# Performance work log

Measured on AMD Instinct MI355X. Metric: run time of the kernel, lower is better.

Reference implementation:

```python
import jax, jax.numpy as jnp
import numpy as np

B, S, D_IN, D_OUT = 4, 2048, 1024, 1024


def setup_inputs() -> dict:
    key = jax.random.key(0)
    kx, kq, kk, kv = jax.random.split(key, 4)
    scale = 1.0 / np.sqrt(D_IN)
    return {
        "x": jax.random.normal(kx, (B, S, D_IN), dtype=jnp.float32),
        "W_q": jax.random.normal(kq, (D_IN, D_OUT), dtype=jnp.float32) * scale,
        "W_k": jax.random.normal(kk, (D_IN, D_OUT), dtype=jnp.float32) * scale,
        "W_v": jax.random.normal(kv, (D_IN, D_OUT), dtype=jnp.float32) * scale,
    }


def reference(x, W_q, W_k, W_v):
    # QKV projections (Linear without bias): [B,S,D_out]
    q = jnp.einsum("bsd,de->bse", x, W_q)
    k = jnp.einsum("bsd,de->bse", x, W_k)
    v = jnp.einsum("bsd,de->bse", x, W_v)

    # Raw scores [B,S,S], causal mask (strict upper triangle -> -inf),
    # then scale by sqrt(d_k) and softmax, matching the torch order of ops.
    scores = jnp.einsum("bqd,bkd->bqk", q, k)
    seq = scores.shape[-1]
    causal = jnp.triu(jnp.ones((seq, seq), dtype=bool), k=1)
    scores = jnp.where(causal[None, :, :], -jnp.inf, scores)
    attn = jax.nn.softmax(scores / jnp.sqrt(jnp.asarray(q.shape[-1], scores.dtype)), axis=-1)
    # dropout p=0.0 -> identity (eval semantics)
    return jnp.einsum("bqk,bkd->bqd", attn, v)
```

## Files before the change

### kernel.cpp

```cpp
#include <hip/hip_runtime.h>

typedef unsigned short u16;
typedef __bf16 bf16x8 __attribute__((ext_vector_type(8)));
typedef float f32x4 __attribute__((ext_vector_type(4)));

__device__ __forceinline__ u16 f2bf(float f) {
    union { float f; unsigned int u; } v; v.f = f;
    unsigned int u = v.u;
    return (u16)((u + 0x7FFFu + ((u >> 16) & 1u)) >> 16);
}

__device__ __forceinline__ void load_lds16(const void* g, void* l) {
    __builtin_amdgcn_global_load_lds(
        (const __attribute__((address_space(1))) unsigned int*)g,
        (__attribute__((address_space(3))) unsigned int*)l,
        16, 0, 0);
}

__global__ void __launch_bounds__(256) prep_kernel(
    const float4* __restrict__ X, u16* __restrict__ xb,
    const float* __restrict__ Wq, const float* __restrict__ Wk,
    const float* __restrict__ Wv,
    u16* __restrict__ Oq, u16* __restrict__ Ok, u16* __restrict__ Ov,
    float* __restrict__ rowsum) {
    __shared__ float tile[32][33];
    const int bid = blockIdx.x, tid = threadIdx.x;
    if (bid < 8192) {
        int idx = bid * 256 + tid;
        float4 v = X[idx];
        ushort4 o;
        o.x = f2bf(v.x); o.y = f2bf(v.y); o.z = f2bf(v.z); o.w = f2bf(v.w);
        *(ushort4*)(xb + (size_t)idx * 4) = o;
    } else if (bid < 11264) {
        int id = bid - 8192;
        int zz = id >> 10;
        const float* W = (zz == 0) ? Wq : (zz == 1) ? Wk : Wv;
        u16* O = (zz == 0) ? Oq : (zz == 1) ? Ok : Ov;
        int n0 = (id & 31) * 32, k0 = ((id >> 5) & 31) * 32;
        int tx = tid & 31, ty = tid >> 5;
        #pragma unroll
        for (int j = 0; j < 32; j += 8)
            tile[ty + j][tx] = W[(size_t)(k0 + ty + j) * 1024 + n0 + tx];
        __syncthreads();
        #pragma unroll
        for (int j = 0; j < 32; j += 8)
            O[(size_t)(n0 + ty + j) * 1024 + k0 + tx] = f2bf(tile[tx][ty + j]);
    } else {
        rowsum[(bid - 11264) * 256 + tid] = 0.f;
    }
}

__global__ void __launch_bounds__(512) gemm_qkv(
    const u16* __restrict__ xb, const u16* __restrict__ WqT,
    const u16* __restrict__ WkT, const u16* __restrict__ WvT,
    u16* __restrict__ Q, u16* __restrict__ Kb, u16* __restrict__ Vt) {

    int L = blockIdx.x;
    int c = L & 7, t = (L >> 3) & 7, hi = L >> 6;
    int p = hi * 8 + c;
    const int z = p >> 6, mtile = p & 63, ntile = t;
    const u16* A = xb;
    const u16* B = (z == 0) ? WqT : (z == 1) ? WkT : WvT;

    __shared__ __align__(16) u16 As[2 * 128 * 32];
    __shared__ __align__(16) u16 Bs[2 * 128 * 32];

    const int tid = threadIdx.x;
    const int lane = tid & 63;
    const int wave = tid >> 6;
    const int wr = wave >> 2, wc = wave & 3;

    const int r0 = tid >> 2;
    const int kb = (((tid & 3) ^ ((r0 >> 1) & 3))) * 16;

    const char* gA = (const char*)(A + (size_t)(mtile * 128 + r0) * 1024) + kb;
    const char* gB = (const char*)(B + (size_t)(ntile * 128 + r0) * 1024) + kb;
    char* lA = (char*)As + tid * 16;
    char* lB = (char*)Bs + tid * 16;

    f32x4 acc[4][2] = {};

    const int quad = lane >> 4;
    const int l16 = lane & 15;
    const int ch = quad ^ ((l16 >> 1) & 3);
    const int aoff = (wr * 64 + l16) * 32 + ch * 8;
    const int boff = (wc * 32 + l16) * 32 + ch * 8;

    for (int kt = 0; kt < 16; ++kt) {
        load_lds16(gA,      lA);
        load_lds16(gA + 64, lA + 8192);
        load_lds16(gB,      lB);
        load_lds16(gB + 64, lB + 8192);
        gA += 128; gB += 128;
        __syncthreads();
        #pragma unroll
        for (int h = 0; h < 2; ++h) {
            const u16* ap = As + h * 4096 + aoff;
            const u16* bp = Bs + h * 4096 + boff;
            bf16x8 af[4], bfv[2];
            #pragma unroll
            for (int r = 0; r < 4; ++r) af[r] = *(const bf16x8*)(ap + r * 512);
            #pragma unroll
            for (int cc = 0; cc < 2; ++cc) bfv[cc] = *(const bf16x8*)(bp + cc * 512);
            #pragma unroll
            for (int r = 0; r < 4; ++r)
                #pragma unroll
                for (int cc = 0; cc < 2; ++cc)
                    acc[r][cc] = __builtin_amdgcn_mfma_f32_16x16x32_bf16(
                        af[r], bfv[cc], acc[r][cc], 0, 0, 0);
        }
        __syncthreads();
    }

    const int grow0 = mtile * 128 + wr * 64 + quad * 4;
    const int gcol0 = ntile * 128 + wc * 32 + l16;

    if (z < 2) {
        u16* C = z ? Kb : Q;
        #pragma unroll
        for (int r = 0; r < 4; ++r)
            #pragma unroll
            for (int cc = 0; cc < 2; ++cc)
                #pragma unroll
                for (int i = 0; i < 4; ++i)
                    C[(size_t)(grow0 + r * 16 + i) * 1024 + gcol0 + cc * 16] =
                        f2bf(acc[r][cc][i]);
    } else {
        #pragma unroll
        for (int r = 0; r < 4; ++r) {
            int m0 = grow0 + r * 16;
            int b = m0 >> 11, s0 = m0 & 2047;
            #pragma unroll
            for (int cc = 0; cc < 2; ++cc) {
                int d = gcol0 + cc * 16;
                ushort4 o;
                o.x = f2bf(acc[r][cc][0]); o.y = f2bf(acc[r][cc][1]);
                o.z = f2bf(acc[r][cc][2]); o.w = f2bf(acc[r][cc][3]);
                *(ushort4*)(Vt + (size_t)b * (1024 * 2048) + (size_t)d * 2048 + s0) = o;
            }
        }
    }
}

__global__ void __launch_bounds__(512) gemm_scores(
    const u16* __restrict__ Q, const u16* __restrict__ Kb,
    u16* __restrict__ S, float* __restrict__ rowsum) {

    const int L = blockIdx.x;
    const int c = L & 7;
    const int q = L >> 3;
    const int z = q / 17;
    const int j = q - z * 17;
    const int mtile = (j <= c) ? c : 15 - c;
    const int ntile = (j <= c) ? j : j - c - 1;

    const u16* A = Q  + (size_t)z * (2048 * 1024);
    const u16* B = Kb + (size_t)z * (2048 * 1024);

    __shared__ __align__(16) u16 As[2 * 128 * 32];
    __shared__ __align__(16) u16 Bs[2 * 128 * 32];

    const int tid = threadIdx.x;
    const int lane = tid & 63;
    const int wave = tid >> 6;
    const int wr = wave >> 2, wc = wave & 3;

    const int r0 = tid >> 2;
    const int kb = (((tid & 3) ^ ((r0 >> 1) & 3))) * 16;

    const char* gA = (const char*)(A + (size_t)(mtile * 128 + r0) * 1024) + kb;
    const char* gB = (const char*)(B + (size_t)(ntile * 128 + r0) * 1024) + kb;
    char* lA = (char*)As + tid * 16;
    char* lB = (char*)Bs + tid * 16;

    f32x4 acc[4][2] = {};

    const int quad = lane >> 4;
    const int l16 = lane & 15;
    const int ch = quad ^ ((l16 >> 1) & 3);
    const int aoff = (wr * 64 + l16) * 32 + ch * 8;
    const int boff = (wc * 32 + l16) * 32 + ch * 8;

    for (int kt = 0; kt < 16; ++kt) {
        load_lds16(gA,      lA);
        load_lds16(gA + 64, lA + 8192);
        load_lds16(gB,      lB);
        load_lds16(gB + 64, lB + 8192);
        gA += 128; gB += 128;
        __syncthreads();
        #pragma unroll
        for (int h = 0; h < 2; ++h) {
            const u16* ap = As + h * 4096 + aoff;
            const u16* bp = Bs + h * 4096 + boff;
            bf16x8 af[4], bfv[2];
            #pragma unroll
            for (int r = 0; r < 4; ++r) af[r] = *(const bf16x8*)(ap + r * 512);
            #pragma unroll
            for (int cc = 0; cc < 2; ++cc) bfv[cc] = *(const bf16x8*)(bp + cc * 512);
            #pragma unroll
            for (int r = 0; r < 4; ++r)
                #pragma unroll
                for (int cc = 0; cc < 2; ++cc)
                    acc[r][cc] = __builtin_amdgcn_mfma_f32_16x16x32_bf16(
                        af[r], bfv[cc], acc[r][cc], 0, 0, 0);
        }
        __syncthreads();
    }

    const int grow0 = mtile * 128 + wr * 64 + quad * 4;
    const int gcol0 = ntile * 128 + wc * 32 + l16;

    u16* C = S + (size_t)z * (2048 * 2048);
    float* rs = rowsum + z * 2048;
    const bool diag = (ntile == mtile);
    float rsum[4][4];
    #pragma unroll
    for (int r = 0; r < 4; ++r)
        #pragma unroll
        for (int i = 0; i < 4; ++i) rsum[r][i] = 0.f;
    #pragma unroll
    for (int r = 0; r < 4; ++r)
        #pragma unroll
        for (int cc = 0; cc < 2; ++cc)
            #pragma unroll
            for (int i = 0; i < 4; ++i) {
                int grow = grow0 + r * 16 + i;
                int gcol = gcol0 + cc * 16;
                float e = 0.f;
                if (!diag || gcol <= grow)
                    e = __expf(acc[r][cc][i] * 0.03125f - 12.0f);
                C[(size_t)grow * 2048 + gcol] = f2bf(e);
                rsum[r][i] += e;
            }
    #pragma unroll
    for (int r = 0; r < 4; ++r)
        #pragma unroll
        for (int i = 0; i < 4; ++i) {
            float s = rsum[r][i];
            s += __shfl_xor(s, 1, 64);
            s += __shfl_xor(s, 2, 64);
            s += __shfl_xor(s, 4, 64);
            s += __shfl_xor(s, 8, 64);
            if (l16 == 0)
                atomicAdd(&rs[grow0 + r * 16 + i], s);
        }
}

__global__ void __launch_bounds__(512) gemm_pv(
    const u16* __restrict__ S, const u16* __restrict__ Vt,
    const float* __restrict__ rowsum, float* __restrict__ out) {

    const int L = blockIdx.x;
    const int ntile = L & 7;
    const int x = L >> 3;
    const int z = x & 3;
    const int mp = x >> 2;

    const u16* Abase = S  + (size_t)z * (2048 * 2048);
    const u16* B     = Vt + (size_t)z * (1024 * 2048);
    const float* rs  = rowsum + z * 2048;
    float* C = out + (size_t)z * (2048 * 1024);

    __shared__ __align__(16) u16 As[2 * 128 * 32];
    __shared__ __align__(16) u16 Bs[2 * 128 * 32];

    const int tid = threadIdx.x;
    const int lane = tid & 63;
    const int wave = tid >> 6;
    const int wr = wave >> 2, wc = wave & 3;

    const int r0 = tid >> 2;
    const int kb = (((tid & 3) ^ ((r0 >> 1) & 3))) * 16;

    char* lA = (char*)As + tid * 16;
    char* lB = (char*)Bs + tid * 16;

    const int quad = lane >> 4;
    const int l16 = lane & 15;
    const int ch = quad ^ ((l16 >> 1) & 3);
    const int aoff = (wr * 64 + l16) * 32 + ch * 8;
    const int boff = (wc * 32 + l16) * 32 + ch * 8;

    #pragma unroll
    for (int ti = 0; ti < 2; ++ti) {
        const int mtile = ti ? mp : 15 - mp;
        const int kiters = (mtile + 1) * 2;

        const char* gA = (const char*)(Abase + (size_t)(mtile * 128 + r0) * 2048) + kb;
        const char* gB = (const char*)(B + (size_t)(ntile * 128 + r0) * 2048) + kb;

        f32x4 acc[4][2] = {};

        for (int kt = 0; kt < kiters; ++kt) {
            load_lds16(gA,      lA);
            load_lds16(gA + 64, lA + 8192);
            load_lds16(gB,      lB);
            load_lds16(gB + 64, lB + 8192);
            gA += 128; gB += 128;
            __syncthreads();
            #pragma unroll
            for (int h = 0; h < 2; ++h) {
                const u16* ap = As + h * 4096 + aoff;
                const u16* bp = Bs + h * 4096 + boff;
                bf16x8 af[4], bfv[2];
                #pragma unroll
                for (int r = 0; r < 4; ++r) af[r] = *(const bf16x8*)(ap + r * 512);
                #pragma unroll
                for (int cc = 0; cc < 2; ++cc) bfv[cc] = *(const bf16x8*)(bp + cc * 512);
                #pragma unroll
                for (int r = 0; r < 4; ++r)
                    #pragma unroll
                    for (int cc = 0; cc < 2; ++cc)
                        acc[r][cc] = __builtin_amdgcn_mfma_f32_16x16x32_bf16(
                            af[r], bfv[cc], acc[r][cc], 0, 0, 0);
            }
            __syncthreads();
        }

        const int grow0 = mtile * 128 + wr * 64 + quad * 4;
        const int gcol0 = ntile * 128 + wc * 32 + l16;
        #pragma unroll
        for (int r = 0; r < 4; ++r)
            #pragma unroll
            for (int i = 0; i < 4; ++i) {
                int grow = grow0 + r * 16 + i;
                float inv = 1.0f / rs[grow];
                #pragma unroll
                for (int cc = 0; cc < 2; ++cc)
                    C[(size_t)grow * 1024 + gcol0 + cc * 16] = acc[r][cc][i] * inv;
            }
    }
}

extern "C" void kernel_launch(void* const* d_in, const int* in_sizes, int n_in,
                              void* d_out, int out_size, void* d_ws, size_t ws_size,
                              hipStream_t stream) {
    const float* x  = (const float*)d_in[0];
    const float* Wq = (const float*)d_in[1];
    const float* Wk = (const float*)d_in[2];
    const float* Wv = (const float*)d_in[3];
    float* out = (float*)d_out;
    char* ws = (char*)d_ws;
    const size_t Mi = 1u << 20;

    u16* xb  = (u16*)(ws);
    u16* WqT = (u16*)(ws + 16 * Mi);
    u16* WkT = (u16*)(ws + 18 * Mi);
    u16* WvT = (u16*)(ws + 20 * Mi);
    u16* Q   = (u16*)(ws + 22 * Mi);
    u16* Kb  = (u16*)(ws + 38 * Mi);
    u16* Vt  = (u16*)(ws + 54 * Mi);
    u16* S   = (u16*)(ws + 70 * Mi);
    float* rowsum = (float*)(ws + 102 * Mi);

    prep_kernel<<<11296, 256, 0, stream>>>(
        (const float4*)x, xb, Wq, Wk, Wv, WqT, WkT, WvT, rowsum);

    gemm_qkv<<<1536, 512, 0, stream>>>(xb, WqT, WkT, WvT, Q, Kb, Vt);

    gemm_scores<<<544, 512, 0, stream>>>(Q, Kb, S, rowsum);

    gemm_pv<<<256, 512, 0, stream>>>(S, Vt, rowsum, out);
}
```

Measured before the change: 225.1 us.

## Split score and PV GEMMs into 128x64 tiles with heavy-first causal scheduling

Both attention GEMMs now use 256-thread blocks that each compute a 128x64 output tile, replacing 512-thread blocks with 128x128 tiles. This raises the block count from 544/256 to 1088/1024. The PV kernel no longer pairs a short and a long causal row-tile in one block; it launches one block per tile, ordered from the longest K range down, so the hardware scheduler balances the load. The aim is better CU occupancy and less tail imbalance, at the cost of reloading each A tile twice and extra per-block overhead.

```diff
diff --git a/kernel.cpp b/kernel.cpp
--- a/kernel.cpp
+++ b/kernel.cpp
@@ -142,34 +142,36 @@
     }
 }
 
-__global__ void __launch_bounds__(512) gemm_scores(
+__global__ void __launch_bounds__(256) gemm_scores(
     const u16* __restrict__ Q, const u16* __restrict__ Kb,
     u16* __restrict__ S, float* __restrict__ rowsum) {
 
     const int L = blockIdx.x;
     const int c = L & 7;
     const int q = L >> 3;
-    const int z = q / 17;
-    const int j = q - z * 17;
-    const int mtile = (j <= c) ? c : 15 - c;
-    const int ntile = (j <= c) ? j : j - c - 1;
+    const int z = q / 34;
+    const int j = q - z * 34;
+    int mtile, nh;
+    if (j < 2 * (c + 1)) { mtile = c;      nh = j; }
+    else                 { mtile = 15 - c; nh = j - 2 * (c + 1); }
 
     const u16* A = Q  + (size_t)z * (2048 * 1024);
     const u16* B = Kb + (size_t)z * (2048 * 1024);
 
     __shared__ __align__(16) u16 As[2 * 128 * 32];
-    __shared__ __align__(16) u16 Bs[2 * 128 * 32];
+    __shared__ __align__(16) u16 Bs[2 * 64 * 32];
 
     const int tid = threadIdx.x;
     const int lane = tid & 63;
     const int wave = tid >> 6;
-    const int wr = wave >> 2, wc = wave & 3;
+    const int wr = wave >> 1, wc = wave & 1;
 
     const int r0 = tid >> 2;
     const int kb = (((tid & 3) ^ ((r0 >> 1) & 3))) * 16;
 
-    const char* gA = (const char*)(A + (size_t)(mtile * 128 + r0) * 1024) + kb;
-    const char* gB = (const char*)(B + (size_t)(ntile * 128 + r0) * 1024) + kb;
+    const char* gA0 = (const char*)(A + (size_t)(mtile * 128 + r0) * 1024) + kb;
+    const char* gA1 = gA0 + (size_t)64 * 1024 * 2;
+    const char* gB  = (const char*)(B + (size_t)(nh * 64 + r0) * 1024) + kb;
     char* lA = (char*)As + tid * 16;
     char* lB = (char*)Bs + tid * 16;
 
@@ -182,16 +184,18 @@
     const int boff = (wc * 32 + l16) * 32 + ch * 8;
 
     for (int kt = 0; kt < 16; ++kt) {
-        load_lds16(gA,      lA);
-        load_lds16(gA + 64, lA + 8192);
-        load_lds16(gB,      lB);
-        load_lds16(gB + 64, lB + 8192);
-        gA += 128; gB += 128;
+        #pragma unroll
+        for (int h = 0; h < 2; ++h) {
+            load_lds16(gA0 + h * 64, lA + h * 8192);
+            load_lds16(gA1 + h * 64, lA + 4096 + h * 8192);
+            load_lds16(gB  + h * 64, lB + h * 4096);
+        }
+        gA0 += 128; gA1 += 128; gB += 128;
         __syncthreads();
         #pragma unroll
         for (int h = 0; h < 2; ++h) {
             const u16* ap = As + h * 4096 + aoff;
-            const u16* bp = Bs + h * 4096 + boff;
+            const u16* bp = Bs + h * 2048 + boff;
             bf16x8 af[4], bfv[2];
             #pragma unroll
             for (int r = 0; r < 4; ++r) af[r] = *(const bf16x8*)(ap + r * 512);
@@ -208,11 +212,10 @@
     }
 
     const int grow0 = mtile * 128 + wr * 64 + quad * 4;
-    const int gcol0 = ntile * 128 + wc * 32 + l16;
+    const int gcol0 = nh * 64 + wc * 32 + l16;
 
     u16* C = S + (size_t)z * (2048 * 2048);
     float* rs = rowsum + z * 2048;
-    const bool diag = (ntile == mtile);
     float rsum[4][4];
     #pragma unroll
     for (int r = 0; r < 4; ++r)
@@ -226,9 +229,9 @@
             for (int i = 0; i < 4; ++i) {
                 int grow = grow0 + r * 16 + i;
                 int gcol = gcol0 + cc * 16;
-                float e = 0.f;
-                if (!diag || gcol <= grow)
-                    e = __expf(acc[r][cc][i] * 0.03125f - 12.0f);
+                float e = (gcol <= grow)
+                              ? __expf(acc[r][cc][i] * 0.03125f - 12.0f)
+                              : 0.f;
                 C[(size_t)grow * 2048 + gcol] = f2bf(e);
                 rsum[r][i] += e;
             }
@@ -246,34 +249,42 @@
         }
 }
 
-__global__ void __launch_bounds__(512) gemm_pv(
+__global__ void __launch_bounds__(256) gemm_pv(
     const u16* __restrict__ S, const u16* __restrict__ Vt,
     const float* __restrict__ rowsum, float* __restrict__ out) {
 
     const int L = blockIdx.x;
-    const int ntile = L & 7;
-    const int x = L >> 3;
-    const int z = x & 3;
-    const int mp = x >> 2;
-
-    const u16* Abase = S  + (size_t)z * (2048 * 2048);
-    const u16* B     = Vt + (size_t)z * (1024 * 2048);
-    const float* rs  = rowsum + z * 2048;
+    const int c = L & 7;
+    const int z = c >> 1;
+    const int nhhi = c & 1;
+    const int j = L >> 3;
+    const int mtile = 15 - (j >> 3);
+    const int nh = nhhi * 8 + (j & 7);
+    const int kiters = (mtile + 1) * 2;
+
+    const u16* A = S  + (size_t)z * (2048 * 2048);
+    const u16* B = Vt + (size_t)z * (1024 * 2048);
+    const float* rs = rowsum + z * 2048;
     float* C = out + (size_t)z * (2048 * 1024);
 
     __shared__ __align__(16) u16 As[2 * 128 * 32];
-    __shared__ __align__(16) u16 Bs[2 * 128 * 32];
+    __shared__ __align__(16) u16 Bs[2 * 64 * 32];
 
     const int tid = threadIdx.x;
     const int lane = tid & 63;
     const int wave = tid >> 6;
-    const int wr = wave >> 2, wc = wave & 3;
+    const int wr = wave >> 1, wc = wave & 1;
 
     const int r0 = tid >> 2;
     const int kb = (((tid & 3) ^ ((r0 >> 1) & 3))) * 16;
 
+    const char* gA0 = (const char*)(A + (size_t)(mtile * 128 + r0) * 2048) + kb;
+    const char* gA1 = gA0 + (size_t)64 * 2048 * 2;
+    const char* gB  = (const char*)(B + (size_t)(nh * 64 + r0) * 2048) + kb;
     char* lA = (char*)As + tid * 16;
     char* lB = (char*)Bs + tid * 16;
+
+    f32x4 acc[4][2] = {};
 
     const int quad = lane >> 4;
     const int l16 = lane & 15;
@@ -281,55 +292,46 @@
     const int aoff = (wr * 64 + l16) * 32 + ch * 8;
     const int boff = (wc * 32 + l16) * 32 + ch * 8;
 
-    #pragma unroll
-    for (int ti = 0; ti < 2; ++ti) {
-        const int mtile = ti ? mp : 15 - mp;
-        const int kiters = (mtile + 1) * 2;
-
-        const char* gA = (const char*)(Abase + (size_t)(mtile * 128 + r0) * 2048) + kb;
-        const char* gB = (const char*)(B + (size_t)(ntile * 128 + r0) * 2048) + kb;
-
-        f32x4 acc[4][2] = {};
-
-        for (int kt = 0; kt < kiters; ++kt) {
-            load_lds16(gA,      lA);
-            load_lds16(gA + 64, lA + 8192);
-            load_lds16(gB,      lB);
-            load_lds16(gB + 64, lB + 8192);
-            gA += 128; gB += 128;
-            __syncthreads();
-            #pragma unroll
-            for (int h = 0; h < 2; ++h) {
-                const u16* ap = As + h * 4096 + aoff;
-                const u16* bp = Bs + h * 4096 + boff;
-                bf16x8 af[4], bfv[2];
-                #pragma unroll
-                for (int r = 0; r < 4; ++r) af[r] = *(const bf16x8*)(ap + r * 512);
-                #pragma unroll
-                for (int cc = 0; cc < 2; ++cc) bfv[cc] = *(const bf16x8*)(bp + cc * 512);
-                #pragma unroll
-                for (int r = 0; r < 4; ++r)
-                    #pragma unroll
-                    for (int cc = 0; cc < 2; ++cc)
-                        acc[r][cc] = __builtin_amdgcn_mfma_f32_16x16x32_bf16(
-                            af[r], bfv[cc], acc[r][cc], 0, 0, 0);
-            }
-            __syncthreads();
-        }
-
-        const int grow0 = mtile * 128 + wr * 64 + quad * 4;
-        const int gcol0 = ntile * 128 + wc * 32 + l16;
-        #pragma unroll
-        for (int r = 0; r < 4; ++r)
-            #pragma unroll
-            for (int i = 0; i < 4; ++i) {
-                int grow = grow0 + r * 16 + i;
-                float inv = 1.0f / rs[grow];
+    for (int kt = 0; kt < kiters; ++kt) {
+        #pragma unroll
+        for (int h = 0; h < 2; ++h) {
+            load_lds16(gA0 + h * 64, lA + h * 8192);
+            load_lds16(gA1 + h * 64, lA + 4096 + h * 8192);
+            load_lds16(gB  + h * 64, lB + h * 4096);
+        }
+        gA0 += 128; gA1 += 128; gB += 128;
+        __syncthreads();
+        #pragma unroll
+        for (int h = 0; h < 2; ++h) {
+            const u16* ap = As + h * 4096 + aoff;
+            const u16* bp = Bs + h * 2048 + boff;
+            bf16x8 af[4], bfv[2];
+            #pragma unroll
+            for (int r = 0; r < 4; ++r) af[r] = *(const bf16x8*)(ap + r * 512);
+            #pragma unroll
+            for (int cc = 0; cc < 2; ++cc) bfv[cc] = *(const bf16x8*)(bp + cc * 512);
+            #pragma unroll
+            for (int r = 0; r < 4; ++r)
                 #pragma unroll
                 for (int cc = 0; cc < 2; ++cc)
-                    C[(size_t)grow * 1024 + gcol0 + cc * 16] = acc[r][cc][i] * inv;
-            }
-    }
+                    acc[r][cc] = __builtin_amdgcn_mfma_f32_16x16x32_bf16(
+                        af[r], bfv[cc], acc[r][cc], 0, 0, 0);
+        }
+        __syncthreads();
+    }
+
+    const int grow0 = mtile * 128 + wr * 64 + quad * 4;
+    const int gcol0 = nh * 64 + wc * 32 + l16;
+    #pragma unroll
+    for (int r = 0; r < 4; ++r)
+        #pragma unroll
+        for (int i = 0; i < 4; ++i) {
+            int grow = grow0 + r * 16 + i;
+            float inv = 1.0f / rs[grow];
+            #pragma unroll
+            for (int cc = 0; cc < 2; ++cc)
+                C[(size_t)grow * 1024 + gcol0 + cc * 16] = acc[r][cc][i] * inv;
+        }
 }
 
 extern "C" void kernel_launch(void* const* d_in, const int* in_sizes, int n_in,
@@ -358,7 +360,7 @@
 
     gemm_qkv<<<1536, 512, 0, stream>>>(xb, WqT, WkT, WvT, Q, Kb, Vt);
 
-    gemm_scores<<<544, 512, 0, stream>>>(Q, Kb, S, rowsum);
-
-    gemm_pv<<<256, 512, 0, stream>>>(S, Vt, rowsum, out);
-}
+    gemm_scores<<<1088, 256, 0, stream>>>(Q, Kb, S, rowsum);
+
+    gemm_pv<<<1024, 256, 0, stream>>>(S, Vt, rowsum, out);
+}
```

Result: slower. 232.4 us (+3.2%).

## Move V projection into the scores kernel to balance launch work

Applied to the files above, without the earlier changes.

The V projection tiles are split out of the QKV GEMM and launched in the same grid as the causal score GEMM, so a single launch covers 544 score tiles plus 512 V tiles. The goal is to fill the GPU better, since the score kernel alone has only 544 blocks and a ragged tail, and to shrink the first GEMM. The cost is a heterogeneous kernel with branches on block type. Scores still depend on Q and K from the previous launch, which the ordering keeps intact.

```diff
diff --git a/kernel.cpp b/kernel.cpp
--- a/kernel.cpp
+++ b/kernel.cpp
@@ -50,17 +50,17 @@
     }
 }
 
-__global__ void __launch_bounds__(512) gemm_qkv(
+__global__ void __launch_bounds__(512) gemm_qk(
     const u16* __restrict__ xb, const u16* __restrict__ WqT,
-    const u16* __restrict__ WkT, const u16* __restrict__ WvT,
-    u16* __restrict__ Q, u16* __restrict__ Kb, u16* __restrict__ Vt) {
+    const u16* __restrict__ WkT,
+    u16* __restrict__ Q, u16* __restrict__ Kb) {
 
     int L = blockIdx.x;
     int c = L & 7, t = (L >> 3) & 7, hi = L >> 6;
     int p = hi * 8 + c;
     const int z = p >> 6, mtile = p & 63, ntile = t;
     const u16* A = xb;
-    const u16* B = (z == 0) ? WqT : (z == 1) ? WkT : WvT;
+    const u16* B = z ? WkT : WqT;
 
     __shared__ __align__(16) u16 As[2 * 128 * 32];
     __shared__ __align__(16) u16 Bs[2 * 128 * 32];
@@ -115,17 +115,101 @@
     const int grow0 = mtile * 128 + wr * 64 + quad * 4;
     const int gcol0 = ntile * 128 + wc * 32 + l16;
 
-    if (z < 2) {
-        u16* C = z ? Kb : Q;
-        #pragma unroll
-        for (int r = 0; r < 4; ++r)
-            #pragma unroll
-            for (int cc = 0; cc < 2; ++cc)
-                #pragma unroll
-                for (int i = 0; i < 4; ++i)
-                    C[(size_t)(grow0 + r * 16 + i) * 1024 + gcol0 + cc * 16] =
-                        f2bf(acc[r][cc][i]);
+    u16* C = z ? Kb : Q;
+    #pragma unroll
+    for (int r = 0; r < 4; ++r)
+        #pragma unroll
+        for (int cc = 0; cc < 2; ++cc)
+            #pragma unroll
+            for (int i = 0; i < 4; ++i)
+                C[(size_t)(grow0 + r * 16 + i) * 1024 + gcol0 + cc * 16] =
+                    f2bf(acc[r][cc][i]);
+}
+
+__global__ void __launch_bounds__(512) gemm_vs(
+    const u16* __restrict__ xb, const u16* __restrict__ WvT,
+    const u16* __restrict__ Q, const u16* __restrict__ Kb,
+    u16* __restrict__ Vt, u16* __restrict__ S,
+    float* __restrict__ rowsum) {
+
+    const int L = blockIdx.x;
+    const bool isV = (L >= 544);
+    int mtile, ntile, z;
+    const u16 *A, *B;
+
+    if (!isV) {
+        const int c = L & 7;
+        const int q = L >> 3;
+        z = q / 17;
+        const int j = q - z * 17;
+        mtile = (j <= c) ? c : 15 - c;
+        ntile = (j <= c) ? j : j - c - 1;
+        A = Q  + (size_t)z * (2048 * 1024);
+        B = Kb + (size_t)z * (2048 * 1024);
     } else {
+        const int id = L - 544;
+        const int c = id & 7, t = (id >> 3) & 7, hi = id >> 6;
+        mtile = hi * 8 + c;
+        ntile = t;
+        z = 0;
+        A = xb;
+        B = WvT;
+    }
+
+    __shared__ __align__(16) u16 As[2 * 128 * 32];
+    __shared__ __align__(16) u16 Bs[2 * 128 * 32];
+
+    const int tid = threadIdx.x;
+    const int lane = tid & 63;
+    const int wave = tid >> 6;
+    const int wr = wave >> 2, wc = wave & 3;
+
+    const int r0 = tid >> 2;
+    const int kb = (((tid & 3) ^ ((r0 >> 1) & 3))) * 16;
+
+    const char* gA = (const char*)(A + (size_t)(mtile * 128 + r0) * 1024) + kb;
+    const char* gB = (const char*)(B + (size_t)(ntile * 128 + r0) * 1024) + kb;
+    char* lA = (char*)As + tid * 16;
+    char* lB = (char*)Bs + tid * 16;
+
+    f32x4 acc[4][2] = {};
+
+    const int quad = lane >> 4;
+    const int l16 = lane & 15;
+    const int ch = quad ^ ((l16 >> 1) & 3);
+    const int aoff = (wr * 64 + l16) * 32 + ch * 8;
+    const int boff = (wc * 32 + l16) * 32 + ch * 8;
+
+    for (int kt = 0; kt < 16; ++kt) {
+        load_lds16(gA,      lA);
+        load_lds16(gA + 64, lA + 8192);
+        load_lds16(gB,      lB);
+        load_lds16(gB + 64, lB + 8192);
+        gA += 128; gB += 128;
+        __syncthreads();
+        #pragma unroll
+        for (int h = 0; h < 2; ++h) {
+            const u16* ap = As + h * 4096 + aoff;
+            const u16* bp = Bs + h * 4096 + boff;
+            bf16x8 af[4], bfv[2];
+            #pragma unroll
+            for (int r = 0; r < 4; ++r) af[r] = *(const bf16x8*)(ap + r * 512);
+            #pragma unroll
+            for (int cc = 0; cc < 2; ++cc) bfv[cc] = *(const bf16x8*)(bp + cc * 512);
+            #pragma unroll
+            for (int r = 0; r < 4; ++r)
+                #pragma unroll
+                for (int cc = 0; cc < 2; ++cc)
+                    acc[r][cc] = __builtin_amdgcn_mfma_f32_16x16x32_bf16(
+                        af[r], bfv[cc], acc[r][cc], 0, 0, 0);
+        }
+        __syncthreads();
+    }
+
+    const int grow0 = mtile * 128 + wr * 64 + quad * 4;
+    const int gcol0 = ntile * 128 + wc * 32 + l16;
+
+    if (isV) {
         #pragma unroll
         for (int r = 0; r < 4; ++r) {
             int m0 = grow0 + r * 16;
@@ -139,111 +223,42 @@
                 *(ushort4*)(Vt + (size_t)b * (1024 * 2048) + (size_t)d * 2048 + s0) = o;
             }
         }
-    }
-}
-
-__global__ void __launch_bounds__(512) gemm_scores(
-    const u16* __restrict__ Q, const u16* __restrict__ Kb,
-    u16* __restrict__ S, float* __restrict__ rowsum) {
-
-    const int L = blockIdx.x;
-    const int c = L & 7;
-    const int q = L >> 3;
-    const int z = q / 17;
-    const int j = q - z * 17;
-    const int mtile = (j <= c) ? c : 15 - c;
-    const int ntile = (j <= c) ? j : j - c - 1;
-
-    const u16* A = Q  + (size_t)z * (2048 * 1024);
-    const u16* B = Kb + (size_t)z * (2048 * 1024);
-
-    __shared__ __align__(16) u16 As[2 * 128 * 32];
-    __shared__ __align__(16) u16 Bs[2 * 128 * 32];
-
-    const int tid = threadIdx.x;
-    const int lane = tid & 63;
-    const int wave = tid >> 6;
-    const int wr = wave >> 2, wc = wave & 3;
-
-    const int r0 = tid >> 2;
-    const int kb = (((tid & 3) ^ ((r0 >> 1) & 3))) * 16;
-
-    const char* gA = (const char*)(A + (size_t)(mtile * 128 + r0) * 1024) + kb;
-    const char* gB = (const char*)(B + (size_t)(ntile * 128 + r0) * 1024) + kb;
-    char* lA = (char*)As + tid * 16;
-    char* lB = (char*)Bs + tid * 16;
-
-    f32x4 acc[4][2] = {};
-
-    const int quad = lane >> 4;
-    const int l16 = lane & 15;
-    const int ch = quad ^ ((l16 >> 1) & 3);
-    const int aoff = (wr * 64 + l16) * 32 + ch * 8;
-    const int boff = (wc * 32 + l16) * 32 + ch * 8;
-
-    for (int kt = 0; kt < 16; ++kt) {
-        load_lds16(gA,      lA);
-        load_lds16(gA + 64, lA + 8192);
-        load_lds16(gB,      lB);
-        load_lds16(gB + 64, lB + 8192);
-        gA += 128; gB += 128;
-        __syncthreads();
-        #pragma unroll
-        for (int h = 0; h < 2; ++h) {
-            const u16* ap = As + h * 4096 + aoff;
-            const u16* bp = Bs + h * 4096 + boff;
-            bf16x8 af[4], bfv[2];
-            #pragma unroll
-            for (int r = 0; r < 4; ++r) af[r] = *(const bf16x8*)(ap + r * 512);
-            #pragma unroll
-            for (int cc = 0; cc < 2; ++cc) bfv[cc] = *(const bf16x8*)(bp + cc * 512);
-            #pragma unroll
-            for (int r = 0; r < 4; ++r)
-                #pragma unroll
-                for (int cc = 0; cc < 2; ++cc)
-                    acc[r][cc] = __builtin_amdgcn_mfma_f32_16x16x32_bf16(
-                        af[r], bfv[cc], acc[r][cc], 0, 0, 0);
-        }
-        __syncthreads();
-    }
-
-    const int grow0 = mtile * 128 + wr * 64 + quad * 4;
-    const int gcol0 = ntile * 128 + wc * 32 + l16;
-
-    u16* C = S + (size_t)z * (2048 * 2048);
-    float* rs = rowsum + z * 2048;
-    const bool diag = (ntile == mtile);
-    float rsum[4][4];
-    #pragma unroll
-    for (int r = 0; r < 4; ++r)
-        #pragma unroll
-        for (int i = 0; i < 4; ++i) rsum[r][i] = 0.f;
-    #pragma unroll
-    for (int r = 0; r < 4; ++r)
-        #pragma unroll
-        for (int cc = 0; cc < 2; ++cc)
+    } else {
+        u16* C = S + (size_t)z * (2048 * 2048);
+        float* rs = rowsum + z * 2048;
+        const bool diag = (ntile == mtile);
+        float rsum[4][4];
+        #pragma unroll
+        for (int r = 0; r < 4; ++r)
+            #pragma unroll
+            for (int i = 0; i < 4; ++i) rsum[r][i] = 0.f;
+        #pragma unroll
+        for (int r = 0; r < 4; ++r)
+            #pragma unroll
+            for (int cc = 0; cc < 2; ++cc)
+                #pragma unroll
+                for (int i = 0; i < 4; ++i) {
+                    int grow = grow0 + r * 16 + i;
+                    int gcol = gcol0 + cc * 16;
+                    float e = 0.f;
+                    if (!diag || gcol <= grow)
+                        e = __expf(acc[r][cc][i] * 0.03125f - 12.0f);
+                    C[(size_t)grow * 2048 + gcol] = f2bf(e);
+                    rsum[r][i] += e;
+                }
+        #pragma unroll
+        for (int r = 0; r < 4; ++r)
             #pragma unroll
             for (int i = 0; i < 4; ++i) {
-                int grow = grow0 + r * 16 + i;
-                int gcol = gcol0 + cc * 16;
-                float e = 0.f;
-                if (!diag || gcol <= grow)
-                    e = __expf(acc[r][cc][i] * 0.03125f - 12.0f);
-                C[(size_t)grow * 2048 + gcol] = f2bf(e);
-                rsum[r][i] += e;
+                float s = rsum[r][i];
+                s += __shfl_xor(s, 1, 64);
+                s += __shfl_xor(s, 2, 64);
+                s += __shfl_xor(s, 4, 64);
+                s += __shfl_xor(s, 8, 64);
+                if (l16 == 0)
+                    atomicAdd(&rs[grow0 + r * 16 + i], s);
             }
-    #pragma unroll
-    for (int r = 0; r < 4; ++r)
-        #pragma unroll
-        for (int i = 0; i < 4; ++i) {
-            float s = rsum[r][i];
-            s += __shfl_xor(s, 1, 64);
-            s += __shfl_xor(s, 2, 64);
-            s += __shfl_xor(s, 4, 64);
-            s += __shfl_xor(s, 8, 64);
-            if (l16 == 0)
-                atomicAdd(&rs[grow0 + r * 16 + i], s);
-        }
+    }
 }
 
 __global__ void __launch_bounds__(512) gemm_pv(
@@ -356,9 +371,9 @@
     prep_kernel<<<11296, 256, 0, stream>>>(
         (const float4*)x, xb, Wq, Wk, Wv, WqT, WkT, WvT, rowsum);
 
-    gemm_qkv<<<1536, 512, 0, stream>>>(xb, WqT, WkT, WvT, Q, Kb, Vt);
-
-    gemm_scores<<<544, 512, 0, stream>>>(Q, Kb, S, rowsum);
+    gemm_qk<<<1024, 512, 0, stream>>>(xb, WqT, WkT, Q, Kb);
+
+    gemm_vs<<<1056, 512, 0, stream>>>(xb, WvT, Q, Kb, Vt, S, rowsum);
 
     gemm_pv<<<256, 512, 0, stream>>>(S, Vt, rowsum, out);
 }
```

Result: no change. 225.7 us (+0.3%).
